# Performance work log

Measured on AMD Instinct MI355X. Metric: run time of the kernel, lower is better.

The kernel has to match this reference:

```python
import jax, jax.numpy as jnp
import numpy as np

B, T, C, H = 2, 2048, 1024, 16
HD = C // H  # 64


def _rope(x, cos, sin):
    # x: [B, T, H, HD]; cos/sin: [T, HD//2]
    xr = x.reshape(*x.shape[:-1], HD // 2, 2)
    xre, xim = xr[..., 0], xr[..., 1]
    c = cos[None, :, None, :]
    s = sin[None, :, None, :]
    out_re = xre * c - xim * s
    out_im = xre * s + xim * c
    return jnp.stack([out_re, out_im], axis=-1).reshape(x.shape)


def setup_inputs() -> dict:
    key = jax.random.key(0)
    ks = jax.random.split(key, 4)
    x = jax.random.normal(ks[0], (B, T, C), dtype=jnp.float32)
    W_qkv = jax.random.normal(ks[1], (3 * C, C), dtype=jnp.float32) * (C ** -0.5)
    W_proj = jax.random.normal(ks[2], (C, C), dtype=jnp.float32) * (C ** -0.5)
    b_proj = jnp.zeros((C,), dtype=jnp.float32)
    # standard RoPE frequencies, theta=10000
    inv_freq = 1.0 / (10000.0 ** (np.arange(0, HD, 2, dtype=np.float32) / HD))
    angles = np.outer(np.arange(T, dtype=np.float32), inv_freq)  # [T, HD/2]
    freqs_cos = jnp.asarray(np.cos(angles), dtype=jnp.float32)
    freqs_sin = jnp.asarray(np.sin(angles), dtype=jnp.float32)
    return {"x": x, "freqs_cos": freqs_cos, "freqs_sin": freqs_sin,
            "W_qkv": W_qkv, "W_proj": W_proj, "b_proj": b_proj}


def reference(x, freqs_cos, freqs_sin, W_qkv, W_proj, b_proj):
    qkv = x @ W_qkv.T                       # [B, T, 3C]
    q, k, v = jnp.split(qkv, 3, axis=-1)
    q = q.reshape(B, T, H, HD)
    k = k.reshape(B, T, H, HD)
    v = v.reshape(B, T, H, HD)
    q = _rope(q, freqs_cos, freqs_sin)
    k = _rope(k, freqs_cos, freqs_sin)
    # [B, H, T, HD]
    q = q.transpose(0, 2, 1, 3)
    k = k.transpose(0, 2, 1, 3)
    v = v.transpose(0, 2, 1, 3)
    att = jnp.einsum('bhqd,bhkd->bhqk', q, k) * (HD ** -0.5)
    causal = jnp.tril(jnp.ones((T, T), dtype=bool))
    att = jnp.where(causal[None, None], att, -jnp.inf)
    att = jax.nn.softmax(att, axis=-1)
    out = jnp.einsum('bhqk,bhkd->bhqd', att, v)
    out = out.transpose(0, 2, 1, 3).reshape(B, T, C)
    return out @ W_proj.T + b_proj
```

## Files before the change

kernel.cpp:

```cpp
#include <hip/hip_runtime.h>


typedef short  bf16x8 __attribute__((ext_vector_type(8)));
typedef float  f32x4  __attribute__((ext_vector_type(4)));
typedef unsigned short u16x4 __attribute__((ext_vector_type(4)));

#define B_  2
#define T_  2048
#define H_  16
#define HD_ 64
#define NINF (-__builtin_inff())

static __device__ __forceinline__ unsigned short f2bf(float f) {
    union { float f; unsigned u; } v; v.f = f;
    unsigned r = v.u + 0x7fffu + ((v.u >> 16) & 1u);
    return (unsigned short)(r >> 16);
}

#define GLOAD_LDS16(gp, lp)                                                              \
    __builtin_amdgcn_global_load_lds((const __attribute__((address_space(1))) void*)(gp), \
                                     (__attribute__((address_space(3))) void*)(lp), 16, 0, 0)

__global__ void convert2(const float* __restrict__ x, const float* __restrict__ wqkv,
                         unsigned short* __restrict__ xb, unsigned short* __restrict__ wqkvb) {
    int i = blockIdx.x * blockDim.x + threadIdx.x;
    const float* src; unsigned short* dst; int off;
    if (i < 1048576) { src = x;    dst = xb;    off = i; }
    else             { src = wqkv; dst = wqkvb; off = i - 1048576; }
    float4 f = ((const float4*)src)[off];
    u16x4 o; o[0] = f2bf(f.x); o[1] = f2bf(f.y); o[2] = f2bf(f.z); o[3] = f2bf(f.w);
    ((u16x4*)dst)[off] = o;
}

__global__ __launch_bounds__(256) void gemm_qkv(const unsigned short* __restrict__ A,
                                                const unsigned short* __restrict__ Bm,
                                                const float* __restrict__ fa,
                                                const float* __restrict__ fb,
                                                unsigned short* __restrict__ Qo,
                                                unsigned short* __restrict__ Ko,
                                                unsigned short* __restrict__ Vt,
                                                const float* __restrict__ wproj,
                                                unsigned short* __restrict__ wprojb) {
    __shared__ __align__(16) unsigned short As[128 * 64];
    __shared__ __align__(16) unsigned short Bs[128 * 64];
    const int bid = blockIdx.x;
    if (bid >= 768) {
        int base = (bid - 768) * 256 + threadIdx.x;
#pragma unroll
        for (int k = 0; k < 16; k++) {
            int u = base + k * 16384;
            float4 f = ((const float4*)wproj)[u];
            u16x4 o; o[0] = f2bf(f.x); o[1] = f2bf(f.y); o[2] = f2bf(f.z); o[3] = f2bf(f.w);
            ((u16x4*)wprojb)[u] = o;
        }
        return;
    }

    const int K = 1024;
    const int tid  = threadIdx.x;
    const int w    = tid >> 6;
    const int lane = tid & 63;
    const int r    = lane & 15, g = lane >> 4;

    const int xcd  = bid & 7;
    const int i_   = bid >> 3;
    const int m0   = ((xcd >> 1) * 8 + i_ / 12) * 128;
    const int n0   = ((xcd & 1) * 12 + i_ % 12) * 128;
    const int wm   = (w >> 1) * 64, wn = (w & 1) * 64;

    f32x4 acc[4][4];
#pragma unroll
    for (int i = 0; i < 4; i++)
#pragma unroll
        for (int j = 0; j < 4; j++) acc[i][j] = (f32x4){0.f, 0.f, 0.f, 0.f};

    const int rowS = tid >> 3;
    const int csS  = (tid & 7) ^ (rowS & 7);
    const int t8e  = tid * 8;
    const unsigned short* ga = A  + (size_t)(m0 + rowS) * K + csS * 8;
    const unsigned short* gb = Bm + (size_t)(n0 + rowS) * K + csS * 8;

    int roff[4][2];
#pragma unroll
    for (int mi = 0; mi < 4; mi++)
#pragma unroll
        for (int kk = 0; kk < 2; kk++)
            roff[mi][kk] = (mi * 16 + r) * 64 + (((4 * kk + g) ^ (r & 7)) * 8);

    for (int k0 = 0; k0 < K; k0 += 64) {
        __syncthreads();
        GLOAD_LDS16(ga + k0,            &As[t8e]);
        GLOAD_LDS16(ga + 32 * K + k0,   &As[2048 + t8e]);
        GLOAD_LDS16(ga + 64 * K + k0,   &As[4096 + t8e]);
        GLOAD_LDS16(ga + 96 * K + k0,   &As[6144 + t8e]);
        GLOAD_LDS16(gb + k0,            &Bs[t8e]);
        GLOAD_LDS16(gb + 32 * K + k0,   &Bs[2048 + t8e]);
        GLOAD_LDS16(gb + 64 * K + k0,   &Bs[4096 + t8e]);
        GLOAD_LDS16(gb + 96 * K + k0,   &Bs[6144 + t8e]);
        __syncthreads();

#pragma unroll
        for (int kk = 0; kk < 2; kk++) {
            bf16x8 a[4], b[4];
#pragma unroll
            for (int mi = 0; mi < 4; mi++) a[mi] = *(const bf16x8*)&As[wm * 64 + roff[mi][kk]];
#pragma unroll
            for (int ni = 0; ni < 4; ni++) b[ni] = *(const bf16x8*)&Bs[wn * 64 + roff[ni][kk]];
#pragma unroll
            for (int mi = 0; mi < 4; mi++)
#pragma unroll
                for (int ni = 0; ni < 4; ni++)
                    acc[mi][ni] = __builtin_amdgcn_mfma_f32_16x16x32_bf16(a[mi], b[ni], acc[mi][ni], 0, 0, 0);
        }
    }

    const float* fcos = (fa[0] > 0.5f) ? fa : fb;
    const float* fsin = (fa[0] > 0.5f) ? fb : fa;
    const int region = n0 >> 10;

    if (region < 2) {
        unsigned short* dst = region ? Ko : Qo;
        const float sgn = (r & 1) ? 1.f : -1.f;
#pragma unroll
        for (int mi = 0; mi < 4; mi++) {
            int row0 = m0 + wm + mi * 16 + 4 * g;
            int b    = row0 >> 11;
            int t0   = row0 & 2047;
#pragma unroll
            for (int ni = 0; ni < 4; ni++) {
                int nn = (n0 & 1023) + wn + ni * 16 + r;
                int h  = nn >> 6, dd = nn & 63;
                int i  = dd >> 1;
                size_t obase = ((size_t)((b * 16 + h) * 2048 + t0)) * 64 + dd;
#pragma unroll
                for (int j = 0; j < 4; j++) {
                    float c = fcos[(t0 + j) * 32 + i];
                    float s = fsin[(t0 + j) * 32 + i];
                    float v  = acc[mi][ni][j];
                    float vp = __shfl_xor(v, 1);
                    float out = __builtin_fmaf(sgn * vp, s, v * c);
                    dst[obase + (size_t)j * 64] = f2bf(out);
                }
            }
        }
    } else {
#pragma unroll
        for (int mi = 0; mi < 4; mi++) {
            int row0 = m0 + wm + mi * 16 + 4 * g;
            int b    = row0 >> 11;
            int t0   = row0 & 2047;
            int tp   = (t0 & ~31) + 8 * ((t0 & 15) >> 2) + 4 * ((t0 & 31) >> 4);
#pragma unroll
            for (int ni = 0; ni < 4; ni++) {
                int nn = (n0 & 1023) + wn + ni * 16 + r;
                int h  = nn >> 6, dd = nn & 63;
                u16x4 ov;
#pragma unroll
                for (int j = 0; j < 4; j++) ov[j] = f2bf(acc[mi][ni][j]);
                *(u16x4*)(Vt + ((size_t)((b * 16 + h) * 64 + dd)) * 2048 + tp) = ov;
            }
        }
    }
}

__global__ __launch_bounds__(256) void gemm_nt(const unsigned short* __restrict__ A,
                                               const unsigned short* __restrict__ Bm,
                                               float* __restrict__ Cm,
                                               const float* __restrict__ bias,
                                               int M, int N, int K) {
    __shared__ __align__(16) unsigned short As[128 * 64];
    __shared__ __align__(16) unsigned short Bs[128 * 64];
    const int tid  = threadIdx.x;
    const int w    = tid >> 6;
    const int lane = tid & 63;
    const int r    = lane & 15, g = lane >> 4;

    const int bid  = blockIdx.x;
    const int xcd  = bid & 7;
    const int i_   = bid >> 3;
    const int m0   = ((xcd >> 1) * 8 + (i_ >> 2)) * 128;
    const int n0   = ((xcd & 1) * 4 + (i_ & 3)) * 128;
    const int wm   = (w >> 1) * 64, wn = (w & 1) * 64;

    f32x4 acc[4][4];
#pragma unroll
    for (int i = 0; i < 4; i++)
#pragma unroll
        for (int j = 0; j < 4; j++) acc[i][j] = (f32x4){0.f, 0.f, 0.f, 0.f};

    const int rowS = tid >> 3;
    const int csS  = (tid & 7) ^ (rowS & 7);
    const int t8e  = tid * 8;
    const unsigned short* ga = A  + (size_t)(m0 + rowS) * K + csS * 8;
    const unsigned short* gb = Bm + (size_t)(n0 + rowS) * K + csS * 8;

    int roff[4][2];
#pragma unroll
    for (int mi = 0; mi < 4; mi++)
#pragma unroll
        for (int kk = 0; kk < 2; kk++)
            roff[mi][kk] = (mi * 16 + r) * 64 + (((4 * kk + g) ^ (r & 7)) * 8);

    for (int k0 = 0; k0 < K; k0 += 64) {
        __syncthreads();
        GLOAD_LDS16(ga + k0,            &As[t8e]);
        GLOAD_LDS16(ga + 32 * K + k0,   &As[2048 + t8e]);
        GLOAD_LDS16(ga + 64 * K + k0,   &As[4096 + t8e]);
        GLOAD_LDS16(ga + 96 * K + k0,   &As[6144 + t8e]);
        GLOAD_LDS16(gb + k0,            &Bs[t8e]);
        GLOAD_LDS16(gb + 32 * K + k0,   &Bs[2048 + t8e]);
        GLOAD_LDS16(gb + 64 * K + k0,   &Bs[4096 + t8e]);
        GLOAD_LDS16(gb + 96 * K + k0,   &Bs[6144 + t8e]);
        __syncthreads();

#pragma unroll
        for (int kk = 0; kk < 2; kk++) {
            bf16x8 a[4], b[4];
#pragma unroll
            for (int mi = 0; mi < 4; mi++) a[mi] = *(const bf16x8*)&As[wm * 64 + roff[mi][kk]];
#pragma unroll
            for (int ni = 0; ni < 4; ni++) b[ni] = *(const bf16x8*)&Bs[wn * 64 + roff[ni][kk]];
#pragma unroll
            for (int mi = 0; mi < 4; mi++)
#pragma unroll
                for (int ni = 0; ni < 4; ni++)
                    acc[mi][ni] = __builtin_amdgcn_mfma_f32_16x16x32_bf16(a[mi], b[ni], acc[mi][ni], 0, 0, 0);
        }
    }

#pragma unroll
    for (int mi = 0; mi < 4; mi++) {
        int row = m0 + wm + mi * 16 + 4 * g;
#pragma unroll
        for (int ni = 0; ni < 4; ni++) {
            int col = n0 + wn + ni * 16 + r;
            float bv = bias[col];
#pragma unroll
            for (int j = 0; j < 4; j++)
                Cm[(size_t)(row + j) * N + col] = acc[mi][ni][j] + bv;
        }
    }
}

template <bool DIAG>
static __device__ __forceinline__ void softmax128(const f32x4 s[8], int key0, int qrow,
                                                  float& m, float& l,
                                                  f32x4 o[4], bf16x8 pf[4], int g) {
    const float SCL = 0.125f * 1.4426950408889634f;
    float sv[32];
#pragma unroll
    for (int ks = 0; ks < 8; ks++)
#pragma unroll
        for (int j = 0; j < 4; j++) {
            float x = s[ks][j];
            if (DIAG && (key0 + ks * 16 + 4 * g + j > qrow)) x = NINF;
            sv[ks * 4 + j] = x;
        }
    float t16[16];
#pragma unroll
    for (int i = 0; i < 16; i++) t16[i] = fmaxf(sv[i], sv[i + 16]);
#pragma unroll
    for (int i = 0; i < 8; i++) t16[i] = fmaxf(t16[i], t16[i + 8]);
#pragma unroll
    for (int i = 0; i < 4; i++) t16[i] = fmaxf(t16[i], t16[i + 4]);
    float tm = fmaxf(fmaxf(t16[0], t16[1]), fmaxf(t16[2], t16[3]));
    tm = fmaxf(tm, __shfl_xor(tm, 16));
    tm = fmaxf(tm, __shfl_xor(tm, 32));

    float msc;
    if (__all(tm <= m)) {
        msc = m * SCL;
    } else {
        float mnew  = fmaxf(m, tm);
        float alpha = __builtin_amdgcn_exp2f((m - mnew) * SCL);
        l *= alpha;
#pragma unroll
        for (int ch = 0; ch < 4; ch++) o[ch] *= alpha;
        m = mnew;
        msc = mnew * SCL;
    }
    float p[32];
#pragma unroll
    for (int i = 0; i < 32; i++) p[i] = __builtin_amdgcn_exp2f(__builtin_fmaf(sv[i], SCL, -msc));
    float ps = 0.f;
#pragma unroll
    for (int i = 0; i < 32; i += 4) ps += ((p[i] + p[i + 1]) + (p[i + 2] + p[i + 3]));
    l += ps;
#pragma unroll
    for (int kb = 0; kb < 4; kb++) {
        union { unsigned w[4]; bf16x8 v; } u;
        asm("v_cvt_pk_bf16_f32 %0, %1, %2" : "=v"(u.w[0]) : "v"(p[8 * kb + 0]), "v"(p[8 * kb + 1]));
        asm("v_cvt_pk_bf16_f32 %0, %1, %2" : "=v"(u.w[1]) : "v"(p[8 * kb + 2]), "v"(p[8 * kb + 3]));
        asm("v_cvt_pk_bf16_f32 %0, %1, %2" : "=v"(u.w[2]) : "v"(p[8 * kb + 4]), "v"(p[8 * kb + 5]));
        asm("v_cvt_pk_bf16_f32 %0, %1, %2" : "=v"(u.w[3]) : "v"(p[8 * kb + 6]), "v"(p[8 * kb + 7]));
        pf[kb] = u.v;
    }
}

__global__ __launch_bounds__(256, 2) void attn_fwd(const unsigned short* __restrict__ Q,
                                                   const unsigned short* __restrict__ Kk,
                                                   const unsigned short* __restrict__ Vt,
                                                   unsigned short* __restrict__ O) {
    __shared__ __align__(16) unsigned short Ks[2][8192];
    __shared__ __align__(16) unsigned short Vs[2][8192];

    const int w    = threadIdx.x >> 6;
    const int lane = threadIdx.x & 63;
    const int l15  = lane & 15, g = lane >> 4;

    const int bid = blockIdx.x;
    const int x   = bid & 7;
    const int y   = (bid >> 3) & 31;
    const int q   = bid >> 8;
    const int bh  = x | ((y & 3) << 3);
    const int z   = y >> 2;
    const int r   = (q == 0) ? z : (q == 1) ? 15 - z : (q == 2) ? 16 + z : 31 - z;
    const int b   = bh >> 4, h = bh & 15;

    const unsigned short* Qb = Q  + (size_t)bh * T_ * HD_;
    const unsigned short* Kb = Kk + (size_t)bh * T_ * HD_;
    const unsigned short* Vb = Vt + (size_t)bh * HD_ * T_;

    const int qrow = r * 64 + 16 * w + l15;
    bf16x8 qf0 = *(const bf16x8*)(Qb + (size_t)qrow * 64 + 8 * g);
    bf16x8 qf1 = *(const bf16x8*)(Qb + (size_t)qrow * 64 + 32 + 8 * g);

    f32x4 o[4];
#pragma unroll
    for (int ch = 0; ch < 4; ch++) o[ch] = (f32x4){0, 0, 0, 0};
    float m2 = NINF, lsum = 0.f;

    int koff[8][2];
#pragma unroll
    for (int i = 0; i < 8; i++) {
        int row = 16 * i + l15;
        koff[i][0] = row * 128 + ((g ^ (row & 7)) << 4);
        koff[i][1] = row * 128 + (((4 + g) ^ (row & 7)) << 4);
    }
    int voff[4][4];
#pragma unroll
    for (int ch = 0; ch < 4; ch++) {
        int row = 16 * ch + l15;
#pragma unroll
        for (int kb = 0; kb < 4; kb++)
            voff[ch][kb] = row * 256 + (((kb * 4 + g) ^ (row & 7)) << 4);
    }

    const int t   = threadIdx.x;
    const int rK0 = t >> 3;
    const int csK = (t & 7) ^ (rK0 & 7);
    const int rV0 = t >> 4;
    const int csV = (t & 15) ^ (rV0 & 7);
    const int t8e = t * 8;
    const unsigned short* sK = Kb + (size_t)rK0 * 64 + csK * 8;
    const unsigned short* sV = Vb + (size_t)rV0 * 2048 + csV * 8;

#define STAGE_TILE(bb, key0_)                                                     \
    do {                                                                          \
        GLOAD_LDS16(sK + (size_t)(key0_) * 64,         &Ks[bb][t8e]);             \
        GLOAD_LDS16(sK + (size_t)(key0_) * 64 + 2048,  &Ks[bb][2048 + t8e]);      \
        GLOAD_LDS16(sK + (size_t)(key0_) * 64 + 4096,  &Ks[bb][4096 + t8e]);      \
        GLOAD_LDS16(sK + (size_t)(key0_) * 64 + 6144,  &Ks[bb][6144 + t8e]);      \
        GLOAD_LDS16(sV + (key0_),                      &Vs[bb][t8e]);             \
        GLOAD_LDS16(sV + (key0_) + 32768,              &Vs[bb][2048 + t8e]);      \
        GLOAD_LDS16(sV + (key0_) + 65536,              &Vs[bb][4096 + t8e]);      \
        GLOAD_LDS16(sV + (key0_) + 98304,              &Vs[bb][6144 + t8e]);      \
    } while (0)

    const int ktEnd = r >> 1;
    STAGE_TILE(0, 0);
    __syncthreads();

    for (int kt = 0; kt <= ktEnd; ++kt) {
        const int key0 = kt * 128;
        const int cur  = kt & 1;
        if (kt < ktEnd) STAGE_TILE(cur ^ 1, key0 + 128);

        const char* KsB = (const char*)&Ks[cur][0];
        const char* VsB = (const char*)&Vs[cur][0];

        f32x4 z4 = (f32x4){0, 0, 0, 0};
        f32x4 s[8];
#pragma unroll
        for (int ks = 0; ks < 8; ks++) {
            bf16x8 kf0 = *(const bf16x8*)(KsB + koff[ks][0]);
            bf16x8 kf1 = *(const bf16x8*)(KsB + koff[ks][1]);
            s[ks] = __builtin_amdgcn_mfma_f32_16x16x32_bf16(kf0, qf0, z4, 0, 0, 0);
            s[ks] = __builtin_amdgcn_mfma_f32_16x16x32_bf16(kf1, qf1, s[ks], 0, 0, 0);
        }

        bf16x8 pf[4];
        if (kt == ktEnd) softmax128<true >(s, key0, qrow, m2, lsum, o, pf, g);
        else             softmax128<false>(s, key0, qrow, m2, lsum, o, pf, g);

#pragma unroll
        for (int ch = 0; ch < 4; ch++) {
            bf16x8 v0 = *(const bf16x8*)(VsB + voff[ch][0]);
            bf16x8 v1 = *(const bf16x8*)(VsB + voff[ch][1]);
            bf16x8 v2 = *(const bf16x8*)(VsB + voff[ch][2]);
            bf16x8 v3 = *(const bf16x8*)(VsB + voff[ch][3]);
            o[ch] = __builtin_amdgcn_mfma_f32_16x16x32_bf16(v0, pf[0], o[ch], 0, 0, 0);
            o[ch] = __builtin_amdgcn_mfma_f32_16x16x32_bf16(v1, pf[1], o[ch], 0, 0, 0);
            o[ch] = __builtin_amdgcn_mfma_f32_16x16x32_bf16(v2, pf[2], o[ch], 0, 0, 0);
            o[ch] = __builtin_amdgcn_mfma_f32_16x16x32_bf16(v3, pf[3], o[ch], 0, 0, 0);
        }

        __syncthreads();
    }
#undef STAGE_TILE

    lsum += __shfl_xor(lsum, 16);
    lsum += __shfl_xor(lsum, 32);
    float inv = 1.f / lsum;

    size_t obase = (((size_t)b * T_ + qrow) * H_ + h) * HD_;
#pragma unroll
    for (int ch = 0; ch < 4; ch++) {
        int d0 = 16 * ch + 4 * g;
        u16x4 ov;
#pragma unroll
        for (int jj = 0; jj < 4; jj++) ov[jj] = f2bf(o[ch][jj] * inv);
        *(u16x4*)(O + obase + d0) = ov;
    }
}

extern "C" void kernel_launch(void* const* d_in, const int* in_sizes, int n_in,
                              void* d_out, int out_size, void* d_ws, size_t ws_size,
                              hipStream_t stream) {
    (void)out_size;
    const float *x = nullptr, *wqkv = nullptr, *wproj = nullptr, *bproj = nullptr;
    const float *fa = nullptr, *fb = nullptr;
    for (int i = 0; i < n_in; i++) {
        switch (in_sizes[i]) {
            case 4194304: x     = (const float*)d_in[i]; break;
            case 3145728: wqkv  = (const float*)d_in[i]; break;
            case 1048576: wproj = (const float*)d_in[i]; break;
            case 1024:    bproj = (const float*)d_in[i]; break;
            case 65536:   if (!fa) fa = (const float*)d_in[i]; else fb = (const float*)d_in[i]; break;
            default: break;
        }
    }
    if (!x || !wqkv || !wproj || !bproj || !fa || !fb) return;
    if (ws_size < (size_t)48 * 1024 * 1024) return;

    char* ws = (char*)d_ws;
    const size_t MB = 1024 * 1024;
    unsigned short* xb     = (unsigned short*)(ws);
    unsigned short* wqkvb  = (unsigned short*)(ws + 8  * MB);
    unsigned short* wprojb = (unsigned short*)(ws + 14 * MB);
    unsigned short* qro    = (unsigned short*)(ws + 16 * MB);
    unsigned short* kro    = (unsigned short*)(ws + 24 * MB);
    unsigned short* vt     = (unsigned short*)(ws + 32 * MB);
    unsigned short* oat    = (unsigned short*)(ws + 40 * MB);

    convert2<<<7168, 256, 0, stream>>>(x, wqkv, xb, wqkvb);

    gemm_qkv<<<832, 256, 0, stream>>>(xb, wqkvb, fa, fb, qro, kro, vt, wproj, wprojb);

    attn_fwd<<<1024, 256, 0, stream>>>(qro, kro, vt, oat);

    gemm_nt<<<256, 256, 0, stream>>>(oat, wprojb, (float*)d_out, bproj,
                                     4096, 1024, 1024);
}
```

Measured before the change: 114.9 us.

## Process two 16-row query tiles per wave in attention to reuse K/V loads

```diff
diff --git a/kernel.cpp b/kernel.cpp
--- a/kernel.cpp
+++ b/kernel.cpp
@@ -314,21 +314,24 @@
     const int q   = bid >> 8;
     const int bh  = x | ((y & 3) << 3);
     const int z   = y >> 2;
-    const int r   = (q == 0) ? z : (q == 1) ? 15 - z : (q == 2) ? 16 + z : 31 - z;
+    const int p   = q ? 15 - z : z;
     const int b   = bh >> 4, h = bh & 15;
 
     const unsigned short* Qb = Q  + (size_t)bh * T_ * HD_;
     const unsigned short* Kb = Kk + (size_t)bh * T_ * HD_;
     const unsigned short* Vb = Vt + (size_t)bh * HD_ * T_;
 
-    const int qrow = r * 64 + 16 * w + l15;
-    bf16x8 qf0 = *(const bf16x8*)(Qb + (size_t)qrow * 64 + 8 * g);
-    bf16x8 qf1 = *(const bf16x8*)(Qb + (size_t)qrow * 64 + 32 + 8 * g);
-
-    f32x4 o[4];
-#pragma unroll
-    for (int ch = 0; ch < 4; ch++) o[ch] = (f32x4){0, 0, 0, 0};
-    float m2 = NINF, lsum = 0.f;
+    const int qrowA = p * 128 + 32 * w + l15;
+    const int qrowB = qrowA + 16;
+    bf16x8 qA0 = *(const bf16x8*)(Qb + (size_t)qrowA * 64 + 8 * g);
+    bf16x8 qA1 = *(const bf16x8*)(Qb + (size_t)qrowA * 64 + 32 + 8 * g);
+    bf16x8 qB0 = *(const bf16x8*)(Qb + (size_t)qrowB * 64 + 8 * g);
+    bf16x8 qB1 = *(const bf16x8*)(Qb + (size_t)qrowB * 64 + 32 + 8 * g);
+
+    f32x4 oA[4], oB[4];
+#pragma unroll
+    for (int ch = 0; ch < 4; ch++) { oA[ch] = (f32x4){0,0,0,0}; oB[ch] = (f32x4){0,0,0,0}; }
+    float mA = NINF, lA = 0.f, mB = NINF, lB = 0.f;
 
     int koff[8][2];
 #pragma unroll
@@ -367,31 +370,37 @@
         GLOAD_LDS16(sV + (key0_) + 98304,              &Vs[bb][6144 + t8e]);      \
     } while (0)
 
-    const int ktEnd = r >> 1;
     STAGE_TILE(0, 0);
     __syncthreads();
 
-    for (int kt = 0; kt <= ktEnd; ++kt) {
+    for (int kt = 0; kt <= p; ++kt) {
         const int key0 = kt * 128;
         const int cur  = kt & 1;
-        if (kt < ktEnd) STAGE_TILE(cur ^ 1, key0 + 128);
+        if (kt < p) STAGE_TILE(cur ^ 1, key0 + 128);
 
         const char* KsB = (const char*)&Ks[cur][0];
         const char* VsB = (const char*)&Vs[cur][0];
 
         f32x4 z4 = (f32x4){0, 0, 0, 0};
-        f32x4 s[8];
+        f32x4 sA[8], sB[8];
 #pragma unroll
         for (int ks = 0; ks < 8; ks++) {
             bf16x8 kf0 = *(const bf16x8*)(KsB + koff[ks][0]);
             bf16x8 kf1 = *(const bf16x8*)(KsB + koff[ks][1]);
-            s[ks] = __builtin_amdgcn_mfma_f32_16x16x32_bf16(kf0, qf0, z4, 0, 0, 0);
-            s[ks] = __builtin_amdgcn_mfma_f32_16x16x32_bf16(kf1, qf1, s[ks], 0, 0, 0);
-        }
-
-        bf16x8 pf[4];
-        if (kt == ktEnd) softmax128<true >(s, key0, qrow, m2, lsum, o, pf, g);
-        else             softmax128<false>(s, key0, qrow, m2, lsum, o, pf, g);
+            sA[ks] = __builtin_amdgcn_mfma_f32_16x16x32_bf16(kf0, qA0, z4, 0, 0, 0);
+            sA[ks] = __builtin_amdgcn_mfma_f32_16x16x32_bf16(kf1, qA1, sA[ks], 0, 0, 0);
+            sB[ks] = __builtin_amdgcn_mfma_f32_16x16x32_bf16(kf0, qB0, z4, 0, 0, 0);
+            sB[ks] = __builtin_amdgcn_mfma_f32_16x16x32_bf16(kf1, qB1, sB[ks], 0, 0, 0);
+        }
+
+        bf16x8 pfA[4], pfB[4];
+        if (kt == p) {
+            softmax128<true >(sA, key0, qrowA, mA, lA, oA, pfA, g);
+            softmax128<true >(sB, key0, qrowB, mB, lB, oB, pfB, g);
+        } else {
+            softmax128<false>(sA, key0, qrowA, mA, lA, oA, pfA, g);
+            softmax128<false>(sB, key0, qrowB, mB, lB, oB, pfB, g);
+        }
 
 #pragma unroll
         for (int ch = 0; ch < 4; ch++) {
@@ -399,28 +408,37 @@
             bf16x8 v1 = *(const bf16x8*)(VsB + voff[ch][1]);
             bf16x8 v2 = *(const bf16x8*)(VsB + voff[ch][2]);
             bf16x8 v3 = *(const bf16x8*)(VsB + voff[ch][3]);
-            o[ch] = __builtin_amdgcn_mfma_f32_16x16x32_bf16(v0, pf[0], o[ch], 0, 0, 0);
-            o[ch] = __builtin_amdgcn_mfma_f32_16x16x32_bf16(v1, pf[1], o[ch], 0, 0, 0);
-            o[ch] = __builtin_amdgcn_mfma_f32_16x16x32_bf16(v2, pf[2], o[ch], 0, 0, 0);
-            o[ch] = __builtin_amdgcn_mfma_f32_16x16x32_bf16(v3, pf[3], o[ch], 0, 0, 0);
+            oA[ch] = __builtin_amdgcn_mfma_f32_16x16x32_bf16(v0, pfA[0], oA[ch], 0, 0, 0);
+            oA[ch] = __builtin_amdgcn_mfma_f32_16x16x32_bf16(v1, pfA[1], oA[ch], 0, 0, 0);
+            oA[ch] = __builtin_amdgcn_mfma_f32_16x16x32_bf16(v2, pfA[2], oA[ch], 0, 0, 0);
+            oA[ch] = __builtin_amdgcn_mfma_f32_16x16x32_bf16(v3, pfA[3], oA[ch], 0, 0, 0);
+            oB[ch] = __builtin_amdgcn_mfma_f32_16x16x32_bf16(v0, pfB[0], oB[ch], 0, 0, 0);
+            oB[ch] = __builtin_amdgcn_mfma_f32_16x16x32_bf16(v1, pfB[1], oB[ch], 0, 0, 0);
+            oB[ch] = __builtin_amdgcn_mfma_f32_16x16x32_bf16(v2, pfB[2], oB[ch], 0, 0, 0);
+            oB[ch] = __builtin_amdgcn_mfma_f32_16x16x32_bf16(v3, pfB[3], oB[ch], 0, 0, 0);
         }
 
         __syncthreads();
     }
 #undef STAGE_TILE
 
-    lsum += __shfl_xor(lsum, 16);
-    lsum += __shfl_xor(lsum, 32);
-    float inv = 1.f / lsum;
-
-    size_t obase = (((size_t)b * T_ + qrow) * H_ + h) * HD_;
+    lA += __shfl_xor(lA, 16); lA += __shfl_xor(lA, 32);
+    lB += __shfl_xor(lB, 16); lB += __shfl_xor(lB, 32);
+    float invA = 1.f / lA, invB = 1.f / lB;
+
+    size_t obA = (((size_t)b * T_ + qrowA) * H_ + h) * HD_;
+    size_t obB = (((size_t)b * T_ + qrowB) * H_ + h) * HD_;
 #pragma unroll
     for (int ch = 0; ch < 4; ch++) {
         int d0 = 16 * ch + 4 * g;
-        u16x4 ov;
-#pragma unroll
-        for (int jj = 0; jj < 4; jj++) ov[jj] = f2bf(o[ch][jj] * inv);
-        *(u16x4*)(O + obase + d0) = ov;
+        u16x4 va_, vb_;
+#pragma unroll
+        for (int jj = 0; jj < 4; jj++) {
+            va_[jj] = f2bf(oA[ch][jj] * invA);
+            vb_[jj] = f2bf(oB[ch][jj] * invB);
+        }
+        *(u16x4*)(O + obA + d0) = va_;
+        *(u16x4*)(O + obB + d0) = vb_;
     }
 }
 
@@ -457,7 +475,7 @@
 
     gemm_qkv<<<832, 256, 0, stream>>>(xb, wqkvb, fa, fb, qro, kro, vt, wproj, wprojb);
 
-    attn_fwd<<<1024, 256, 0, stream>>>(qro, kro, vt, oat);
+    attn_fwd<<<512, 256, 0, stream>>>(qro, kro, vt, oat);
 
     gemm_nt<<<256, 256, 0, stream>>>(oat, wprojb, (float*)d_out, bproj,
                                      4096, 1024, 1024);
```

Result: no change. 115.6 us (+0.6%).
